# Kernel optimization log

Hardware: AMD Instinct MI355X
Metric: run time of the kernel (lower is better)

## Reference

```python
import jax, jax.numpy as jnp
import numpy as np

N = 500000      # total nodes
B = 10000       # number of graphs
D = 256         # node_size == global_size
SLOPE = 0.01    # LeakyReLU negative slope (torch default)

def leaky_relu(x):
    return jnp.where(x >= 0, x, SLOPE * x)

def setup_inputs() -> dict:
    key = jax.random.key(0)
    ks = jax.random.split(key, 10)
    xg_old = jax.random.normal(ks[0], (B, D), dtype=jnp.float32)
    x = jax.random.normal(ks[1], (N, D), dtype=jnp.float32)
    batch = jnp.sort(jax.random.randint(ks[2], (N,), 0, B)).astype(jnp.int64)
    s = 1.0 / np.sqrt(D)
    W_gate = jax.random.uniform(ks[3], (D, 1), minval=-s, maxval=s, dtype=jnp.float32)
    b_gate = jax.random.uniform(ks[4], (1,), minval=-s, maxval=s, dtype=jnp.float32)
    W_feat = jax.random.uniform(ks[5], (D, D), minval=-s, maxval=s, dtype=jnp.float32)
    b_feat = jax.random.uniform(ks[6], (D,), minval=-s, maxval=s, dtype=jnp.float32)
    s2 = 1.0 / np.sqrt(2 * D)
    W_t = jax.random.uniform(ks[7], (2 * D, D), minval=-s2, maxval=s2, dtype=jnp.float32)
    b_t = jax.random.uniform(ks[8], (D,), minval=-s2, maxval=s2, dtype=jnp.float32)
    return {"xg_old": xg_old, "x": x, "batch": batch,
            "W_gate": W_gate, "b_gate": b_gate,
            "W_feat": W_feat, "b_feat": b_feat,
            "W_t": W_t, "b_t": b_t}

def reference(xg_old, x, batch, W_gate, b_gate, W_feat, b_feat, W_t, b_t):
    batch = batch.astype(jnp.int32)
    # AttentionalAggregation: per-graph softmax over gate scores, weighted sum of feats
    gate = x @ W_gate + b_gate                               # [N, 1]
    feat = leaky_relu(x @ W_feat + b_feat)                   # [N, D]
    m = jax.ops.segment_max(gate, batch, num_segments=B)     # [B, 1]
    g = jnp.exp(gate - m[batch])                             # stable exp
    s = jax.ops.segment_sum(g, batch, num_segments=B)        # [B, 1]
    alpha = g / s[batch]                                     # [N, 1]
    xg = jax.ops.segment_sum(alpha * feat, batch, num_segments=B)  # [B, D]
    # concat with old global state, transform, residual
    cat = jnp.concatenate([xg, xg_old], axis=1)              # [B, 2D]
    out = leaky_relu(cat @ W_t + b_t) + xg_old               # [B, D]
    return out
```

## Files before the change

kernel.cpp:

```cpp
#include <hip/hip_runtime.h>
#include <hip/hip_bf16.h>
#include <math.h>

#define D 256

typedef short v8s __attribute__((ext_vector_type(8)));
typedef float f32x4 __attribute__((ext_vector_type(4)));

__global__ void segstart_kernel(const int* __restrict__ batch, int* __restrict__ seg_start,
                                int N, int B) {
    int b = blockIdx.x * blockDim.x + threadIdx.x;
    if (b > B) return;
    int lo = 0, hi = N;
    while (lo < hi) {
        int mid = (lo + hi) >> 1;
        if (batch[mid] < b) lo = mid + 1; else hi = mid;
    }
    seg_start[b] = lo;
}

__global__ __launch_bounds__(256) void gate_kernel(const float* __restrict__ x,
                                                   const float* __restrict__ Wg,
                                                   const float* __restrict__ bg,
                                                   float* __restrict__ gate, int N) {
    int wave = threadIdx.x >> 6;
    int lane = threadIdx.x & 63;
    int n = blockIdx.x * 4 + wave;
    if (n >= N) return;
    const float4 xv = *(const float4*)(x + (size_t)n * D + lane * 4);
    const float4 wv = *(const float4*)(Wg + lane * 4);
    float d = xv.x * wv.x + xv.y * wv.y + xv.z * wv.z + xv.w * wv.w;
    #pragma unroll
    for (int off = 32; off > 0; off >>= 1) d += __shfl_down(d, off, 64);
    if (lane == 0) gate[n] = d + bg[0];
}

__global__ __launch_bounds__(256) void stats_kernel(const float* __restrict__ gate,
                                                    const int* __restrict__ seg_start,
                                                    float* __restrict__ mvec,
                                                    float* __restrict__ invs, int B) {
    int wid = blockIdx.x * 4 + (threadIdx.x >> 6);
    int lane = threadIdx.x & 63;
    if (wid >= B) return;
    int s0 = seg_start[wid], s1 = seg_start[wid + 1];
    float m = -INFINITY;
    for (int i = s0 + lane; i < s1; i += 64) m = fmaxf(m, gate[i]);
    #pragma unroll
    for (int off = 32; off > 0; off >>= 1) m = fmaxf(m, __shfl_xor(m, off, 64));
    float s = 0.f;
    for (int i = s0 + lane; i < s1; i += 64) s += __expf(gate[i] - m);
    #pragma unroll
    for (int off = 32; off > 0; off >>= 1) s += __shfl_xor(s, off, 64);
    if (lane == 0) { mvec[wid] = m; invs[wid] = (s > 0.f) ? 1.f / s : 0.f; }
}

__global__ void wconv_kernel(const float* __restrict__ Wf, unsigned short* __restrict__ Wb) {
    int idx = blockIdx.x * 256 + threadIdx.x;
    int k = idx >> 8, n = idx & 255;
    int n_tile = n >> 4, k_step = k >> 5;
    int lane = ((k >> 3) & 3) * 16 + (n & 15);
    int j = k & 7;
    int dst = (((n_tile * 8 + k_step) * 64) + lane) * 8 + j;
    Wb[dst] = __bfloat16_as_ushort(__float2bfloat16(Wf[k * 256 + n]));
}

__global__ __launch_bounds__(256) void feat_attn_kernel(
    const float* __restrict__ x, const unsigned short* __restrict__ Wb,
    const float* __restrict__ bfeat, const float* __restrict__ gate,
    const int* __restrict__ batch, const float* __restrict__ mvec,
    const float* __restrict__ invs, float* __restrict__ xg, int N) {

    __shared__ unsigned short feat_s[64 * 260];
    __shared__ float alpha_s[64];
    __shared__ int batch_s[64];

    const int tid = threadIdx.x;
    const int n0 = blockIdx.x * 64;
    const int cnt = min(64, N - n0);

    if (tid < 64) {
        if (tid < cnt) {
            int n = n0 + tid;
            int b = batch[n];
            batch_s[tid] = b;
            alpha_s[tid] = __expf(gate[n] - mvec[b]) * invs[b];
        } else { batch_s[tid] = -1; alpha_s[tid] = 0.f; }
    }

    const int w = tid >> 6, lane = tid & 63;
    const int mrow = lane & 15, q = lane >> 4;

    f32x4 acc[4][4];
    #pragma unroll
    for (int i = 0; i < 4; i++)
        #pragma unroll
        for (int j = 0; j < 4; j++) acc[i][j] = (f32x4){0.f, 0.f, 0.f, 0.f};

    size_t rowbase[4];
    #pragma unroll
    for (int rb = 0; rb < 4; rb++) {
        int r = n0 + rb * 16 + mrow;
        if (r > N - 1) r = N - 1;
        rowbase[rb] = (size_t)r * D + q * 8;
    }

    for (int ks = 0; ks < 8; ks++) {
        v8s a[4], bfr[4];
        #pragma unroll
        for (int rb = 0; rb < 4; rb++) {
            const float* p = x + rowbase[rb] + ks * 32;
            float4 f0 = *(const float4*)p;
            float4 f1 = *(const float4*)(p + 4);
            v8s v;
            v[0] = (short)__bfloat16_as_ushort(__float2bfloat16(f0.x));
            v[1] = (short)__bfloat16_as_ushort(__float2bfloat16(f0.y));
            v[2] = (short)__bfloat16_as_ushort(__float2bfloat16(f0.z));
            v[3] = (short)__bfloat16_as_ushort(__float2bfloat16(f0.w));
            v[4] = (short)__bfloat16_as_ushort(__float2bfloat16(f1.x));
            v[5] = (short)__bfloat16_as_ushort(__float2bfloat16(f1.y));
            v[6] = (short)__bfloat16_as_ushort(__float2bfloat16(f1.z));
            v[7] = (short)__bfloat16_as_ushort(__float2bfloat16(f1.w));
            a[rb] = v;
        }
        #pragma unroll
        for (int cb = 0; cb < 4; cb++) {
            int nt = w * 4 + cb;
            bfr[cb] = *(const v8s*)(Wb + (((size_t)nt * 8 + ks) * 64 + lane) * 8);
        }
        #pragma unroll
        for (int rb = 0; rb < 4; rb++)
            #pragma unroll
            for (int cb = 0; cb < 4; cb++)
                acc[rb][cb] = __builtin_amdgcn_mfma_f32_16x16x32_bf16(
                    a[rb], bfr[cb], acc[rb][cb], 0, 0, 0);
    }

    #pragma unroll
    for (int cb = 0; cb < 4; cb++) {
        int col = w * 64 + cb * 16 + mrow;
        float bias = bfeat[col];
        #pragma unroll
        for (int rb = 0; rb < 4; rb++) {
            #pragma unroll
            for (int reg = 0; reg < 4; reg++) {
                float y = acc[rb][cb][reg] + bias;
                y = (y >= 0.f) ? y : 0.01f * y;
                feat_s[(rb * 16 + q * 4 + reg) * 260 + col] =
                    __bfloat16_as_ushort(__float2bfloat16(y));
            }
        }
    }
    __syncthreads();

    float sum = 0.f;
    int cur = batch_s[0];
    for (int i = 0; i < cnt; i++) {
        int b = batch_s[i];
        if (b != cur) {
            atomicAdd(&xg[(size_t)cur * D + tid], sum);
            sum = 0.f; cur = b;
        }
        float y = __bfloat162float(__ushort_as_bfloat16(feat_s[i * 260 + tid]));
        sum = fmaf(alpha_s[i], y, sum);
    }
    atomicAdd(&xg[(size_t)cur * D + tid], sum);
}

__global__ __launch_bounds__(256) void out_kernel(
    const float* __restrict__ xg, const float* __restrict__ xg_old,
    const float* __restrict__ Wt, const float* __restrict__ bt,
    float* __restrict__ out) {
    const int t = threadIdx.x;
    const int r0 = blockIdx.x * 8;
    float acc[8];
    #pragma unroll
    for (int r = 0; r < 8; r++) acc[r] = 0.f;

    for (int k = 0; k < D; k++) {
        const float w = Wt[k * D + t];
        #pragma unroll
        for (int r = 0; r < 8; r++)
            acc[r] = fmaf(xg[(size_t)(r0 + r) * D + k], w, acc[r]);
    }
    for (int k = 0; k < D; k++) {
        const float w = Wt[(D + k) * D + t];
        #pragma unroll
        for (int r = 0; r < 8; r++)
            acc[r] = fmaf(xg_old[(size_t)(r0 + r) * D + k], w, acc[r]);
    }
    const float btt = bt[t];
    #pragma unroll
    for (int r = 0; r < 8; r++) {
        float y = acc[r] + btt;
        y = (y >= 0.f) ? y : 0.01f * y;
        out[(size_t)(r0 + r) * D + t] = y + xg_old[(size_t)(r0 + r) * D + t];
    }
}

extern "C" void kernel_launch(void* const* d_in, const int* in_sizes, int n_in,
                              void* d_out, int out_size, void* d_ws, size_t ws_size,
                              hipStream_t stream) {
    const float* xg_old = (const float*)d_in[0];
    const float* x      = (const float*)d_in[1];
    const int*   batch  = (const int*)d_in[2];
    const float* W_gate = (const float*)d_in[3];
    const float* b_gate = (const float*)d_in[4];
    const float* W_feat = (const float*)d_in[5];
    const float* b_feat = (const float*)d_in[6];
    const float* W_t    = (const float*)d_in[7];
    const float* b_t    = (const float*)d_in[8];
    float* out = (float*)d_out;

    const int N = in_sizes[1] / D;
    const int B = in_sizes[0] / D;

    char* ws = (char*)d_ws;
    int*            seg_start = (int*)ws;
    float*          gate      = (float*)(ws + 0x10000);
    float*          mvec      = (float*)(ws + 0x220000);
    float*          invs      = (float*)(ws + 0x230000);
    unsigned short* Wb        = (unsigned short*)(ws + 0x240000);
    float*          xg        = (float*)(ws + 0x280000);

    segstart_kernel<<<(B + 1 + 255) / 256, 256, 0, stream>>>(batch, seg_start, N, B);
    gate_kernel<<<(N + 3) / 4, 256, 0, stream>>>(x, W_gate, b_gate, gate, N);
    stats_kernel<<<(B + 3) / 4, 256, 0, stream>>>(gate, seg_start, mvec, invs, B);
    wconv_kernel<<<256, 256, 0, stream>>>(W_feat, Wb);
    hipMemsetAsync(xg, 0, (size_t)B * D * sizeof(float), stream);
    feat_attn_kernel<<<(N + 63) / 64, 256, 0, stream>>>(
        x, Wb, b_feat, gate, batch, mvec, invs, xg, N);
    out_kernel<<<B / 8, 256, 0, stream>>>(xg, xg_old, W_t, b_t, out);
}
```

Measured before the change: 1.106 ms.

## Fuse gate, softmax and feature aggregation per graph; MFMA output transform

```diff
diff --git a/kernel.cpp b/kernel.cpp
--- a/kernel.cpp
+++ b/kernel.cpp
@@ -6,89 +6,188 @@
 
 typedef short v8s __attribute__((ext_vector_type(8)));
 typedef float f32x4 __attribute__((ext_vector_type(4)));
-
-__global__ void segstart_kernel(const int* __restrict__ batch, int* __restrict__ seg_start,
-                                int N, int B) {
-    int b = blockIdx.x * blockDim.x + threadIdx.x;
-    if (b > B) return;
-    int lo = 0, hi = N;
-    while (lo < hi) {
-        int mid = (lo + hi) >> 1;
-        if (batch[mid] < b) lo = mid + 1; else hi = mid;
-    }
-    seg_start[b] = lo;
-}
-
-__global__ __launch_bounds__(256) void gate_kernel(const float* __restrict__ x,
-                                                   const float* __restrict__ Wg,
-                                                   const float* __restrict__ bg,
-                                                   float* __restrict__ gate, int N) {
-    int wave = threadIdx.x >> 6;
-    int lane = threadIdx.x & 63;
-    int n = blockIdx.x * 4 + wave;
-    if (n >= N) return;
-    const float4 xv = *(const float4*)(x + (size_t)n * D + lane * 4);
-    const float4 wv = *(const float4*)(Wg + lane * 4);
-    float d = xv.x * wv.x + xv.y * wv.y + xv.z * wv.z + xv.w * wv.w;
-    #pragma unroll
-    for (int off = 32; off > 0; off >>= 1) d += __shfl_down(d, off, 64);
-    if (lane == 0) gate[n] = d + bg[0];
-}
-
-__global__ __launch_bounds__(256) void stats_kernel(const float* __restrict__ gate,
-                                                    const int* __restrict__ seg_start,
-                                                    float* __restrict__ mvec,
-                                                    float* __restrict__ invs, int B) {
-    int wid = blockIdx.x * 4 + (threadIdx.x >> 6);
-    int lane = threadIdx.x & 63;
-    if (wid >= B) return;
-    int s0 = seg_start[wid], s1 = seg_start[wid + 1];
-    float m = -INFINITY;
-    for (int i = s0 + lane; i < s1; i += 64) m = fmaxf(m, gate[i]);
-    #pragma unroll
-    for (int off = 32; off > 0; off >>= 1) m = fmaxf(m, __shfl_xor(m, off, 64));
-    float s = 0.f;
-    for (int i = s0 + lane; i < s1; i += 64) s += __expf(gate[i] - m);
-    #pragma unroll
-    for (int off = 32; off > 0; off >>= 1) s += __shfl_xor(s, off, 64);
-    if (lane == 0) { mvec[wid] = m; invs[wid] = (s > 0.f) ? 1.f / s : 0.f; }
-}
-
-__global__ void wconv_kernel(const float* __restrict__ Wf, unsigned short* __restrict__ Wb) {
-    int idx = blockIdx.x * 256 + threadIdx.x;
-    int k = idx >> 8, n = idx & 255;
-    int n_tile = n >> 4, k_step = k >> 5;
-    int lane = ((k >> 3) & 3) * 16 + (n & 15);
-    int j = k & 7;
-    int dst = (((n_tile * 8 + k_step) * 64) + lane) * 8 + j;
-    Wb[dst] = __bfloat16_as_ushort(__float2bfloat16(Wf[k * 256 + n]));
-}
-
-__global__ __launch_bounds__(256) void feat_attn_kernel(
-    const float* __restrict__ x, const unsigned short* __restrict__ Wb,
-    const float* __restrict__ bfeat, const float* __restrict__ gate,
-    const int* __restrict__ batch, const float* __restrict__ mvec,
-    const float* __restrict__ invs, float* __restrict__ xg, int N) {
-
-    __shared__ unsigned short feat_s[64 * 260];
+typedef float f32x16 __attribute__((ext_vector_type(16)));
+
+__device__ __forceinline__ unsigned short f2b(float f) {
+    return __bfloat16_as_ushort(__float2bfloat16(f));
+}
+
+__global__ void prep_kernel(const int* __restrict__ batch, int* __restrict__ seg_start,
+                            const float* __restrict__ Wf, unsigned short* __restrict__ Wb32,
+                            const float* __restrict__ Wt, unsigned short* __restrict__ Wtb,
+                            int N, int B) {
+    const int blk = blockIdx.x, tid = threadIdx.x;
+    if (blk < 40) {
+        int b = blk * 256 + tid;
+        if (b > B) return;
+        int lo = 0, hi = N;
+        while (lo < hi) {
+            int mid = (lo + hi) >> 1;
+            if (batch[mid] < b) lo = mid + 1; else hi = mid;
+        }
+        seg_start[b] = lo;
+    } else if (blk < 296) {
+        int idx = (blk - 40) * 256 + tid;
+        int k = idx >> 8, n = idx & 255;
+        int lane = ((k >> 3) & 1) * 32 + (n & 31);
+        int j = k & 7, kst = k >> 4, ntile = n >> 5;
+        Wb32[(((ntile * 16 + kst) * 64) + lane) * 8 + j] = f2b(Wf[k * 256 + n]);
+    } else {
+        int idx = (blk - 296) * 256 + tid;
+        int k = idx >> 8, n = idx & 255;
+        int ntile = n >> 4, kst = k >> 5;
+        int lane = ((k >> 3) & 3) * 16 + (n & 15);
+        int j = k & 7;
+        Wtb[(((ntile * 16 + kst) * 64) + lane) * 8 + j] = f2b(Wt[k * 256 + n]);
+    }
+}
+
+__global__ __launch_bounds__(256, 3) void fused_graph_kernel(
+    const float* __restrict__ x, const float* __restrict__ Wg,
+    const float* __restrict__ bg, const unsigned short* __restrict__ Wb32,
+    const float* __restrict__ bfeat, const int* __restrict__ seg_start,
+    float* __restrict__ xg, int N) {
+
+    const int b = blockIdx.x;
+    const int s0 = seg_start[b];
+    const int S  = seg_start[b + 1] - s0;
+
+    const int tid = threadIdx.x;
+    const int w = tid >> 6, lane = tid & 63;
+    const int l31 = lane & 31, lh = lane >> 5;
+
     __shared__ float alpha_s[64];
-    __shared__ int batch_s[64];
-
+    __shared__ float shr[2];
+
+    const float bgv = bg[0];
+    const float bias0 = bfeat[(w * 2 + 0) * 32 + l31];
+    const float bias1 = bfeat[(w * 2 + 1) * 32 + l31];
+
+    float m_run = -INFINITY;
+    float s_run = 0.f;
+    float xg_col0 = 0.f, xg_col1 = 0.f;
+
+    for (int c0 = 0; c0 < S; c0 += 64) {
+        const int cnt = min(64, S - c0);
+
+        size_t abase[2];
+        #pragma unroll
+        for (int rt = 0; rt < 2; rt++) {
+            int i = rt * 32 + l31;
+            if (i > cnt - 1) i = cnt - 1;
+            abase[rt] = (size_t)(s0 + c0 + i) * D + lh * 8;
+        }
+
+        f32x16 acc[2][2];
+        #pragma unroll
+        for (int i = 0; i < 2; i++)
+            #pragma unroll
+            for (int j = 0; j < 2; j++)
+                #pragma unroll
+                for (int e = 0; e < 16; e++) acc[i][j][e] = 0.f;
+
+        float gp0 = 0.f, gp1 = 0.f;
+
+        #pragma unroll
+        for (int ks = 0; ks < 16; ks++) {
+            float4 f00 = *(const float4*)(x + abase[0] + ks * 16);
+            float4 f01 = *(const float4*)(x + abase[0] + ks * 16 + 4);
+            float4 f10 = *(const float4*)(x + abase[1] + ks * 16);
+            float4 f11 = *(const float4*)(x + abase[1] + ks * 16 + 4);
+            v8s a0, a1;
+            a0[0]=(short)f2b(f00.x); a0[1]=(short)f2b(f00.y);
+            a0[2]=(short)f2b(f00.z); a0[3]=(short)f2b(f00.w);
+            a0[4]=(short)f2b(f01.x); a0[5]=(short)f2b(f01.y);
+            a0[6]=(short)f2b(f01.z); a0[7]=(short)f2b(f01.w);
+            a1[0]=(short)f2b(f10.x); a1[1]=(short)f2b(f10.y);
+            a1[2]=(short)f2b(f10.z); a1[3]=(short)f2b(f10.w);
+            a1[4]=(short)f2b(f11.x); a1[5]=(short)f2b(f11.y);
+            a1[6]=(short)f2b(f11.z); a1[7]=(short)f2b(f11.w);
+
+            if (w == 0) {
+                float4 wg0 = *(const float4*)(Wg + ks * 16 + lh * 8);
+                float4 wg1 = *(const float4*)(Wg + ks * 16 + lh * 8 + 4);
+                gp0 = fmaf(f00.x, wg0.x, gp0); gp0 = fmaf(f00.y, wg0.y, gp0);
+                gp0 = fmaf(f00.z, wg0.z, gp0); gp0 = fmaf(f00.w, wg0.w, gp0);
+                gp0 = fmaf(f01.x, wg1.x, gp0); gp0 = fmaf(f01.y, wg1.y, gp0);
+                gp0 = fmaf(f01.z, wg1.z, gp0); gp0 = fmaf(f01.w, wg1.w, gp0);
+                gp1 = fmaf(f10.x, wg0.x, gp1); gp1 = fmaf(f10.y, wg0.y, gp1);
+                gp1 = fmaf(f10.z, wg0.z, gp1); gp1 = fmaf(f10.w, wg0.w, gp1);
+                gp1 = fmaf(f11.x, wg1.x, gp1); gp1 = fmaf(f11.y, wg1.y, gp1);
+                gp1 = fmaf(f11.z, wg1.z, gp1); gp1 = fmaf(f11.w, wg1.w, gp1);
+            }
+
+            v8s bf0 = *(const v8s*)(Wb32 + (((size_t)(w * 2 + 0) * 16 + ks) * 64 + lane) * 8);
+            v8s bf1 = *(const v8s*)(Wb32 + (((size_t)(w * 2 + 1) * 16 + ks) * 64 + lane) * 8);
+
+            acc[0][0] = __builtin_amdgcn_mfma_f32_32x32x16_bf16(a0, bf0, acc[0][0], 0, 0, 0);
+            acc[0][1] = __builtin_amdgcn_mfma_f32_32x32x16_bf16(a0, bf1, acc[0][1], 0, 0, 0);
+            acc[1][0] = __builtin_amdgcn_mfma_f32_32x32x16_bf16(a1, bf0, acc[1][0], 0, 0, 0);
+            acc[1][1] = __builtin_amdgcn_mfma_f32_32x32x16_bf16(a1, bf1, acc[1][1], 0, 0, 0);
+        }
+
+        if (w == 0) {
+            gp0 += __shfl_xor(gp0, 32, 64);
+            gp1 += __shfl_xor(gp1, 32, 64);
+            float g0 = (l31 < cnt)      ? gp0 + bgv : -INFINITY;
+            float g1 = (32 + l31 < cnt) ? gp1 + bgv : -INFINITY;
+            float mm = fmaxf(g0, g1);
+            #pragma unroll
+            for (int off = 16; off; off >>= 1) mm = fmaxf(mm, __shfl_xor(mm, off, 64));
+            float m_new = fmaxf(m_run, mm);
+            float scale = __expf(m_run - m_new);
+            m_run = m_new;
+            float a0 = __expf(g0 - m_new);
+            float a1 = __expf(g1 - m_new);
+            float sc = a0 + a1;
+            #pragma unroll
+            for (int off = 16; off; off >>= 1) sc += __shfl_xor(sc, off, 64);
+            if (lh == 0) { alpha_s[l31] = a0; alpha_s[32 + l31] = a1; }
+            if (lane == 0) { shr[0] = scale; shr[1] = sc; }
+        }
+        __syncthreads();
+
+        const float scale = shr[0];
+        const float s_chunk = shr[1];
+        s_run = s_run * scale + s_chunk;
+        xg_col0 *= scale;
+        xg_col1 *= scale;
+
+        #pragma unroll
+        for (int rt = 0; rt < 2; rt++) {
+            #pragma unroll
+            for (int g = 0; g < 4; g++) {
+                #pragma unroll
+                for (int rr = 0; rr < 4; rr++) {
+                    float al = alpha_s[rt * 32 + rr + 8 * g + 4 * lh];
+                    float y0 = acc[rt][0][g * 4 + rr] + bias0;
+                    y0 = (y0 >= 0.f) ? y0 : 0.01f * y0;
+                    xg_col0 = fmaf(al, y0, xg_col0);
+                    float y1 = acc[rt][1][g * 4 + rr] + bias1;
+                    y1 = (y1 >= 0.f) ? y1 : 0.01f * y1;
+                    xg_col1 = fmaf(al, y1, xg_col1);
+                }
+            }
+        }
+        __syncthreads();
+    }
+
+    xg_col0 += __shfl_xor(xg_col0, 32, 64);
+    xg_col1 += __shfl_xor(xg_col1, 32, 64);
+    const float inv = (s_run > 0.f) ? 1.f / s_run : 0.f;
+    if (lh == 0) {
+        xg[(size_t)b * D + (w * 2 + 0) * 32 + l31] = xg_col0 * inv;
+        xg[(size_t)b * D + (w * 2 + 1) * 32 + l31] = xg_col1 * inv;
+    }
+}
+
+__global__ __launch_bounds__(256) void out_mfma_kernel(
+    const float* __restrict__ xg, const float* __restrict__ xg_old,
+    const unsigned short* __restrict__ Wtb, const float* __restrict__ bt,
+    float* __restrict__ out, int B) {
     const int tid = threadIdx.x;
-    const int n0 = blockIdx.x * 64;
-    const int cnt = min(64, N - n0);
-
-    if (tid < 64) {
-        if (tid < cnt) {
-            int n = n0 + tid;
-            int b = batch[n];
-            batch_s[tid] = b;
-            alpha_s[tid] = __expf(gate[n] - mvec[b]) * invs[b];
-        } else { batch_s[tid] = -1; alpha_s[tid] = 0.f; }
-    }
-
-    const int w = tid >> 6, lane = tid & 63;
-    const int mrow = lane & 15, q = lane >> 4;
+    const int w = tid >> 6, lane = tid & 63, mrow = lane & 15, q = lane >> 4;
+    const int r0 = blockIdx.x * 64;
 
     f32x4 acc[4][4];
     #pragma unroll
@@ -99,34 +198,30 @@
     size_t rowbase[4];
     #pragma unroll
     for (int rb = 0; rb < 4; rb++) {
-        int r = n0 + rb * 16 + mrow;
-        if (r > N - 1) r = N - 1;
+        int r = r0 + rb * 16 + mrow;
+        if (r > B - 1) r = B - 1;
         rowbase[rb] = (size_t)r * D + q * 8;
     }
 
-    for (int ks = 0; ks < 8; ks++) {
+    #pragma unroll
+    for (int ks = 0; ks < 16; ks++) {
         v8s a[4], bfr[4];
         #pragma unroll
         for (int rb = 0; rb < 4; rb++) {
-            const float* p = x + rowbase[rb] + ks * 32;
-            float4 f0 = *(const float4*)p;
-            float4 f1 = *(const float4*)(p + 4);
+            const float* src = (ks < 8) ? (xg + rowbase[rb] + ks * 32)
+                                        : (xg_old + rowbase[rb] + (ks - 8) * 32);
+            float4 f0 = *(const float4*)src;
+            float4 f1 = *(const float4*)(src + 4);
             v8s v;
-            v[0] = (short)__bfloat16_as_ushort(__float2bfloat16(f0.x));
-            v[1] = (short)__bfloat16_as_ushort(__float2bfloat16(f0.y));
-            v[2] = (short)__bfloat16_as_ushort(__float2bfloat16(f0.z));
-            v[3] = (short)__bfloat16_as_ushort(__float2bfloat16(f0.w));
-            v[4] = (short)__bfloat16_as_ushort(__float2bfloat16(f1.x));
-            v[5] = (short)__bfloat16_as_ushort(__float2bfloat16(f1.y));
-            v[6] = (short)__bfloat16_as_ushort(__float2bfloat16(f1.z));
-            v[7] = (short)__bfloat16_as_ushort(__float2bfloat16(f1.w));
+            v[0] = (short)f2b(f0.x); v[1] = (short)f2b(f0.y);
+            v[2] = (short)f2b(f0.z); v[3] = (short)f2b(f0.w);
+            v[4] = (short)f2b(f1.x); v[5] = (short)f2b(f1.y);
+            v[6] = (short)f2b(f1.z); v[7] = (short)f2b(f1.w);
             a[rb] = v;
         }
         #pragma unroll
-        for (int cb = 0; cb < 4; cb++) {
-            int nt = w * 4 + cb;
-            bfr[cb] = *(const v8s*)(Wb + (((size_t)nt * 8 + ks) * 64 + lane) * 8);
-        }
+        for (int cb = 0; cb < 4; cb++)
+            bfr[cb] = *(const v8s*)(Wtb + (((size_t)(w * 4 + cb) * 16 + ks) * 64 + lane) * 8);
         #pragma unroll
         for (int rb = 0; rb < 4; rb++)
             #pragma unroll
@@ -138,62 +233,19 @@
     #pragma unroll
     for (int cb = 0; cb < 4; cb++) {
         int col = w * 64 + cb * 16 + mrow;
-        float bias = bfeat[col];
+        float bias = bt[col];
         #pragma unroll
         for (int rb = 0; rb < 4; rb++) {
             #pragma unroll
             for (int reg = 0; reg < 4; reg++) {
-                float y = acc[rb][cb][reg] + bias;
-                y = (y >= 0.f) ? y : 0.01f * y;
-                feat_s[(rb * 16 + q * 4 + reg) * 260 + col] =
-                    __bfloat16_as_ushort(__float2bfloat16(y));
+                int row = r0 + rb * 16 + q * 4 + reg;
+                if (row < B) {
+                    float y = acc[rb][cb][reg] + bias;
+                    y = (y >= 0.f) ? y : 0.01f * y;
+                    out[(size_t)row * D + col] = y + xg_old[(size_t)row * D + col];
+                }
             }
         }
-    }
-    __syncthreads();
-
-    float sum = 0.f;
-    int cur = batch_s[0];
-    for (int i = 0; i < cnt; i++) {
-        int b = batch_s[i];
-        if (b != cur) {
-            atomicAdd(&xg[(size_t)cur * D + tid], sum);
-            sum = 0.f; cur = b;
-        }
-        float y = __bfloat162float(__ushort_as_bfloat16(feat_s[i * 260 + tid]));
-        sum = fmaf(alpha_s[i], y, sum);
-    }
-    atomicAdd(&xg[(size_t)cur * D + tid], sum);
-}
-
-__global__ __launch_bounds__(256) void out_kernel(
-    const float* __restrict__ xg, const float* __restrict__ xg_old,
-    const float* __restrict__ Wt, const float* __restrict__ bt,
-    float* __restrict__ out) {
-    const int t = threadIdx.x;
-    const int r0 = blockIdx.x * 8;
-    float acc[8];
-    #pragma unroll
-    for (int r = 0; r < 8; r++) acc[r] = 0.f;
-
-    for (int k = 0; k < D; k++) {
-        const float w = Wt[k * D + t];
-        #pragma unroll
-        for (int r = 0; r < 8; r++)
-            acc[r] = fmaf(xg[(size_t)(r0 + r) * D + k], w, acc[r]);
-    }
-    for (int k = 0; k < D; k++) {
-        const float w = Wt[(D + k) * D + t];
-        #pragma unroll
-        for (int r = 0; r < 8; r++)
-            acc[r] = fmaf(xg_old[(size_t)(r0 + r) * D + k], w, acc[r]);
-    }
-    const float btt = bt[t];
-    #pragma unroll
-    for (int r = 0; r < 8; r++) {
-        float y = acc[r] + btt;
-        y = (y >= 0.f) ? y : 0.01f * y;
-        out[(size_t)(r0 + r) * D + t] = y + xg_old[(size_t)(r0 + r) * D + t];
     }
 }
 
@@ -216,18 +268,12 @@
 
     char* ws = (char*)d_ws;
     int*            seg_start = (int*)ws;
-    float*          gate      = (float*)(ws + 0x10000);
-    float*          mvec      = (float*)(ws + 0x220000);
-    float*          invs      = (float*)(ws + 0x230000);
-    unsigned short* Wb        = (unsigned short*)(ws + 0x240000);
-    float*          xg        = (float*)(ws + 0x280000);
-
-    segstart_kernel<<<(B + 1 + 255) / 256, 256, 0, stream>>>(batch, seg_start, N, B);
-    gate_kernel<<<(N + 3) / 4, 256, 0, stream>>>(x, W_gate, b_gate, gate, N);
-    stats_kernel<<<(B + 3) / 4, 256, 0, stream>>>(gate, seg_start, mvec, invs, B);
-    wconv_kernel<<<256, 256, 0, stream>>>(W_feat, Wb);
-    hipMemsetAsync(xg, 0, (size_t)B * D * sizeof(float), stream);
-    feat_attn_kernel<<<(N + 63) / 64, 256, 0, stream>>>(
-        x, Wb, b_feat, gate, batch, mvec, invs, xg, N);
-    out_kernel<<<B / 8, 256, 0, stream>>>(xg, xg_old, W_t, b_t, out);
-}
+    unsigned short* Wb32      = (unsigned short*)(ws + 0x10000);
+    unsigned short* Wtb       = (unsigned short*)(ws + 0x30000);
+    float*          xg        = (float*)(ws + 0x70000);
+
+    prep_kernel<<<808, 256, 0, stream>>>(batch, seg_start, W_feat, Wb32, W_t, Wtb, N, B);
+    fused_graph_kernel<<<B, 256, 0, stream>>>(x, W_gate, b_gate, Wb32, b_feat,
+                                              seg_start, xg, N);
+    out_mfma_kernel<<<(B + 63) / 64, 256, 0, stream>>>(xg, xg_old, Wtb, b_t, out, B);
+}
```

New measurement: 1.175 ms. 6.3% more time.
